# Kernel tuning notes

Measured on AMD Instinct MI355X. Metric: run time of the kernel, lower is better.

## Reference

```python
import jax, jax.numpy as jnp
import numpy as np


def _rotate_half(x):
    a, b = jnp.split(x, 2, axis=-1)
    return jnp.concatenate([-b, a], axis=-1)


def _rope_tables(L, d, dtype):
    inv = 1.0 / (10000.0 ** (jnp.arange(0, d, 2, dtype=jnp.float32) / d))
    ang = jnp.arange(L, dtype=jnp.float32)[:, None] * inv[None, :]  # (L, d/2)
    cos = jnp.repeat(jnp.cos(ang), 2, axis=-1)[None, :, None, :].astype(dtype)  # (1,L,1,d)
    sin = jnp.repeat(jnp.sin(ang), 2, axis=-1)[None, :, None, :].astype(dtype)
    return cos, sin


def setup_inputs() -> dict:
    key = jax.random.key(0)
    ks = jax.random.split(key, 7)
    B, L, D, h = 1, 1024, 768, 12
    d = D // h
    s = 0.02
    return {
        "X": jax.random.normal(ks[0], (B, L, D), jnp.float32),
        "Wq": jax.random.normal(ks[1], (D, D), jnp.float32) * s,
        "Wk": jax.random.normal(ks[2], (D, D), jnp.float32) * s,
        "Wv": jax.random.normal(ks[3], (D, D), jnp.float32) * s,
        "Wu": jax.random.normal(ks[4], (D, D), jnp.float32) * s,
        "Wg": jax.random.normal(ks[5], (3 * h, D), jnp.float32) * s,
        "Wo": jax.random.normal(ks[6], (D, D), jnp.float32) * s,
        "prior_mu": jnp.zeros((1, 1, h, d), jnp.float32),
        "prior_log_tau": jnp.zeros((1, 1, h, 1), jnp.float32),
    }


def _forward(X, Wq, Wk, Wv, Wu, Wg, Wo, prior_mu, prior_log_tau):
    B, L, D = X.shape
    h = prior_mu.shape[2]
    d = D // h
    eps = 1e-12
    # projections (torch Linear: x @ W.T, no bias)
    q = (X @ Wq.T).reshape(B, L, h, d)
    k = (X @ Wk.T).reshape(B, L, h, d)
    v = (X @ Wv.T).reshape(B, L, h, d)
    u = (X @ Wu.T).reshape(B, L, h, d)
    gate = (X @ Wg.T).reshape(B, L, h, 3)
    t = jnp.arange(1, L + 1, dtype=X.dtype).reshape(1, L, 1, 1)
    # calculate_logit (logit_type='deviation', causal)
    log_tau = jnp.exp(jnp.clip(prior_log_tau, -50.0, 30.0))
    u_sum = jnp.cumsum(u, axis=1)
    bar_u = (log_tau * prior_mu + u_sum) / (log_tau + t)
    s_i = -jnp.sum(u * bar_u, axis=-1, keepdims=True) / np.float32(np.sqrt(d))  # (B,L,h,1)
    # RoPE + L2 normalize q, k
    cos, sin = _rope_tables(L, d, X.dtype)
    q = q * cos + _rotate_half(q) * sin
    k = k * cos + _rotate_half(k) * sin
    q = q / jnp.maximum(jnp.linalg.norm(q, axis=-1, keepdims=True), eps)
    k = k / jnp.maximum(jnp.linalg.norm(k, axis=-1, keepdims=True), eps)
    # associative causal branch of compute_o
    s_max = jax.lax.stop_gradient(jnp.max(s_i, axis=1, keepdims=True))
    exp_s = jnp.exp(s_i - s_max)              # (B,L,h,1)
    E_t = jnp.cumsum(exp_s, axis=1)
    P_t = jnp.cumsum(s_i, axis=1)
    kv = jnp.einsum('blhd,blhe->blhde', k, v)  # (B,L,h,d,d)
    F_t = jnp.cumsum(exp_s[..., None] * kv, axis=1)
    G_t = jnp.cumsum(s_i[..., None] * kv, axis=1)
    H_t = jnp.cumsum(kv, axis=1)
    sig1 = jax.nn.sigmoid(gate[..., 0:1])      # (B,L,h,1)
    sigh = jax.nn.sigmoid(gate[..., 1:2])
    alpha = sigh / (E_t + eps)
    beta = (sig1 - sigh) / t
    gamma = -((beta * P_t + sigh) / t)
    M = alpha[..., None] * F_t + beta[..., None] * G_t + gamma[..., None] * H_t
    out = jnp.einsum('blhd,blhde->blhe', q, M)  # (B,L,h,d)
    # LayerNorm over head dim, eps=1e-5, no affine
    mu = jnp.mean(out, axis=-1, keepdims=True)
    var = jnp.mean(jnp.square(out - mu), axis=-1, keepdims=True)
    out = (out - mu) / jnp.sqrt(var + 1e-5)
    # output projection (dropout=0.0 -> identity)
    return out.reshape(B, L, D) @ Wo.T


def reference(X, Wq, Wk, Wv, Wu, Wg, Wo, prior_mu, prior_log_tau):
    return _forward(X, Wq, Wk, Wv, Wu, Wg, Wo, prior_mu, prior_log_tau)
```

## Files before the change

kernel.cpp:

```cpp
#include <hip/hip_runtime.h>
#include <hip/hip_bf16.h>
#include <math.h>

typedef __attribute__((ext_vector_type(8))) short bf16x8;
typedef __attribute__((ext_vector_type(4))) float f32x4;

#define SEQ 1024
#define DIM 768
#define NH 12
#define HD 64


__device__ __forceinline__ float wave_reduce_sum(float v) {
    for (int off = 1; off < 64; off <<= 1) v += __shfl_xor(v, off);
    return v;
}
__device__ __forceinline__ short f2bs(float x) {
    __hip_bfloat16 h = __float2bfloat16(x);
    return *reinterpret_cast<short*>(&h);
}
__device__ __forceinline__ float bs2f(short x) {
    __hip_bfloat16 h = *reinterpret_cast<__hip_bfloat16*>(&x);
    return (float)h;
}
__device__ __forceinline__ bf16x8 cvt8r(const float4& a, const float4& b) {
    bf16x8 r;
    r[0]=f2bs(a.x); r[1]=f2bs(a.y); r[2]=f2bs(a.z); r[3]=f2bs(a.w);
    r[4]=f2bs(b.x); r[5]=f2bs(b.y); r[6]=f2bs(b.z); r[7]=f2bs(b.w);
    return r;
}
__device__ __forceinline__ void async_copy16(const void* gptr, void* ldsbase, int lane) {
#if __has_builtin(__builtin_amdgcn_global_load_lds)
    __builtin_amdgcn_global_load_lds(
        (const __attribute__((address_space(1))) unsigned int*)gptr,
        (__attribute__((address_space(3))) unsigned int*)ldsbase, 16, 0, 0);
#else
    *(bf16x8*)((short*)ldsbase + lane*8) = *(const bf16x8*)gptr;
#endif
}

__global__ __launch_bounds__(256) void k_prep(const float* __restrict__ X,
    const float* __restrict__ Wq, const float* __restrict__ Wk,
    const float* __restrict__ Wv, const float* __restrict__ Wu,
    const float* __restrict__ Wg, const float* __restrict__ Wo,
    short* __restrict__ Xb, short* __restrict__ Wqb, short* __restrict__ Wkb,
    short* __restrict__ Wvb, short* __restrict__ Wub, short* __restrict__ Wgb,
    short* __restrict__ Wob)
{
    int seg = blockIdx.y;
    const float* src; short* dst; int n8;
    switch (seg) {
        case 0: src = X;  dst = Xb;  n8 = 98304; break;
        case 1: src = Wq; dst = Wqb; n8 = 73728; break;
        case 2: src = Wk; dst = Wkb; n8 = 73728; break;
        case 3: src = Wv; dst = Wvb; n8 = 73728; break;
        case 4: src = Wu; dst = Wub; n8 = 73728; break;
        case 5: src = Wg; dst = Wgb; n8 = 3456;  break;
        default: src = Wo; dst = Wob; n8 = 73728; break;
    }
    int i = blockIdx.x*256 + threadIdx.x;
    if (i >= n8) return;
    const float* s = src + (size_t)i*8;
    *(bf16x8*)(dst + (size_t)i*8) = cvt8r(*(const float4*)s, *(const float4*)(s + 4));
}

__global__ __launch_bounds__(256, 4) void k_proj5(const short* __restrict__ Xb,
    const short* __restrict__ Wqb, const short* __restrict__ Wkb,
    const short* __restrict__ Wvb, const short* __restrict__ Wub,
    const short* __restrict__ Wgb,
    __hip_bfloat16* __restrict__ Qb, __hip_bfloat16* __restrict__ Kb,
    __hip_bfloat16* __restrict__ Vt, __hip_bfloat16* __restrict__ Ub,
    float* __restrict__ G)
{
    int t = blockIdx.x;
    int mat, rt, ct;
    if (t < 576)      { int m3 = t/192; mat = (m3==2)?3:m3; int r = t%192; rt = r/12; ct = r%12; }
    else if (t < 768) { mat = 2; int r = t-576; rt = r/16; ct = r%16; }
    else              { mat = 4; rt = t-768; ct = 0; }

    __shared__ short lds[16384];

    int tid = threadIdx.x;
    int wv = tid>>6, lane = tid&63, g = lane>>4, n = lane&15;
    int wm = wv>>1, wn = wv&1;

    const short* Asrc; const short* Bsrc; int arow0, brow0, Brows;
    if (mat == 2) { Asrc = Wvb; Bsrc = Xb; arow0 = rt*64; brow0 = ct*64; Brows = SEQ; }
    else {
        Asrc = Xb; arow0 = rt*64; brow0 = ct*64;
        Bsrc = (mat==0)?Wqb:(mat==1)?Wkb:(mat==3)?Wub:Wgb;
        Brows = (mat==4) ? 36 : DIM;
    }

    auto dma_step = [&](int buf, int k0) {
        short* Ab = lds + buf*4096;
        short* Bb = lds + 8192 + buf*4096;
        for (int p = 0; p < 2; ++p) {
            int sbase = p*256 + wv*64;
            int s = sbase + lane;
            int r = s >> 3, c = s & 7, cl = c ^ (r & 7);
            async_copy16(Asrc + (size_t)(arow0 + r)*DIM + k0 + cl*8, Ab + sbase*8, lane);
            int gr = brow0 + r; if (gr >= Brows) gr = Brows - 1;
            async_copy16(Bsrc + (size_t)gr*DIM + k0 + cl*8, Bb + sbase*8, lane);
        }
    };

    f32x4 acc[2][2];
    for (int i=0;i<2;++i) for (int j=0;j<2;++j) acc[i][j] = (f32x4){0,0,0,0};

    dma_step(0, 0);
    for (int it = 0; it < 12; ++it) {
        __syncthreads();
        if (it < 11) dma_step(1 - (it & 1), (it + 1)*64);
        int buf = it & 1;
        const short* Ab = lds + buf*4096;
        const short* Bb = lds + 8192 + buf*4096;
        for (int ks = 0; ks < 2; ++ks) {
            int q = ks*4 + g;
            bf16x8 af[2], bfr[2];
            for (int i=0;i<2;++i)
                af[i] = *(const bf16x8*)(&Ab[((wm*32+i*16+n)*8 + (q ^ (n&7)))*8]);
            for (int j=0;j<2;++j)
                bfr[j] = *(const bf16x8*)(&Bb[((wn*32+j*16+n)*8 + (q ^ (n&7)))*8]);
            for (int i=0;i<2;++i)
                for (int j=0;j<2;++j)
                    acc[i][j] = __builtin_amdgcn_mfma_f32_16x16x32_bf16(af[i], bfr[j], acc[i][j], 0,0,0);
        }
    }
    __syncthreads();

    if (mat == 4) {
        for (int i=0;i<2;++i) for (int j=0;j<2;++j) for (int r=0;r<4;++r) {
            int row = rt*64 + wm*32 + i*16 + g*4 + r;
            int col = wn*32 + j*16 + n;
            if (col < 36) G[(size_t)row*36 + col] = acc[i][j][r];
        }
        return;
    }

    short* C = lds;
    for (int i=0;i<2;++i) for (int j=0;j<2;++j) for (int r=0;r<4;++r)
        C[(wm*32 + i*16 + g*4 + r)*64 + wn*32 + j*16 + n] = f2bs(acc[i][j][r]);
    __syncthreads();

    if (mat == 2) {
        const unsigned int* Cu = (const unsigned int*)C;
        for (int k = 0; k < 8; ++k) {
            int idx = k*256 + tid;
            int row = idx >> 5, cu = idx & 31;
            ((unsigned int*)(Vt + (size_t)(rt*64 + row)*SEQ + ct*64))[cu] = Cu[row*32 + cu];
        }
    } else if (mat == 3) {
        const unsigned int* Cu = (const unsigned int*)C;
        for (int k = 0; k < 8; ++k) {
            int idx = k*256 + tid;
            int row = idx >> 5, cu = idx & 31;
            ((unsigned int*)(Ub + ((size_t)ct*SEQ + rt*64 + row)*HD))[cu] = Cu[row*32 + cu];
        }
    } else {
        __hip_bfloat16* dst = (mat==0) ? Qb : Kb;
        int i2 = lane >> 1;
        float inv = expf((float)i2 * (-9.210340371976184f / 32.f));
        float c0, s0, C1, S1;
        sincosf((float)(rt*64 + wv*16) * inv, &s0, &c0);
        sincosf(inv, &S1, &C1);
        for (int k = 0; k < 16; ++k) {
            int row = wv*16 + k;
            int l = rt*64 + row;
            float x = bs2f(C[row*64 + lane]);
            float p = __shfl(x, lane ^ 32);
            float rot = (lane < 32) ? -p : p;
            float y = x*c0 + rot*s0;
            float nrm = wave_reduce_sum(y*y);
            y = y / fmaxf(sqrtf(nrm), 1e-12f);
            dst[((size_t)ct*SEQ + l)*HD + lane] = __float2bfloat16(y);
            float cn = c0*C1 - s0*S1;
            s0 = s0*C1 + c0*S1;
            c0 = cn;
        }
    }
}

__global__ __launch_bounds__(256) void k_si(const __hip_bfloat16* __restrict__ Ub,
    const float* __restrict__ pmu, const float* __restrict__ plt,
    float* __restrict__ si_)
{
    int T = blockIdx.x, h = blockIdx.y;
    int wv = threadIdx.x >> 6, lane = threadIdx.x & 63;
    int g = lane >> 4, n = lane & 15;
    int lbase = T*16;
    const short* ub = (const short*)Ub + (size_t)h*SEQ*HD;
    __shared__ float pbuf[4][16];

    bf16x8 a0 = *(const bf16x8*)(ub + (size_t)(lbase + n)*HD + g*8);
    bf16x8 a1 = *(const bf16x8*)(ub + (size_t)(lbase + n)*HD + 32 + g*8);

    float p[4] = {0.f, 0.f, 0.f, 0.f};

    for (int jt = wv; jt < T; jt += 4) {
        const short* br = ub + (size_t)(jt*16 + n)*HD + g*8;
        bf16x8 b0 = *(const bf16x8*)br;
        bf16x8 b1 = *(const bf16x8*)(br + 32);
        f32x4 sacc = {0.f,0.f,0.f,0.f};
        sacc = __builtin_amdgcn_mfma_f32_16x16x32_bf16(a0, b0, sacc, 0,0,0);
        sacc = __builtin_amdgcn_mfma_f32_16x16x32_bf16(a1, b1, sacc, 0,0,0);
        for (int r = 0; r < 4; ++r) p[r] += sacc[r];
    }
    if (wv == 0) {
        const short* br = ub + (size_t)(lbase + n)*HD + g*8;
        bf16x8 b0 = *(const bf16x8*)br;
        bf16x8 b1 = *(const bf16x8*)(br + 32);
        f32x4 d = {0.f,0.f,0.f,0.f};
        d = __builtin_amdgcn_mfma_f32_16x16x32_bf16(a0, b0, d, 0,0,0);
        d = __builtin_amdgcn_mfma_f32_16x16x32_bf16(a1, b1, d, 0,0,0);
        for (int r = 0; r < 4; ++r) if (n <= g*4 + r) p[r] += d[r];
    }
    if (wv == 1) {
        float ltau = expf(fminf(fmaxf(plt[h], -50.f), 30.f));
        for (int r = 0; r < 4; ++r) {
            int l = lbase + g*4 + r;
            float acc = 0.f;
            for (int c = n; c < 64; c += 16)
                acc += bs2f(ub[(size_t)l*HD + c]) * pmu[h*HD + c];
            p[r] += ltau * acc;
        }
    }
    for (int off = 1; off < 16; off <<= 1)
        for (int r = 0; r < 4; ++r) p[r] += __shfl_xor(p[r], off);
    if (n == 0)
        for (int r = 0; r < 4; ++r) pbuf[wv][g*4 + r] = p[r];
    __syncthreads();
    if (wv == 0 && n == 0) {
        float ltau = expf(fminf(fmaxf(plt[h], -50.f), 30.f));
        for (int r = 0; r < 4; ++r) {
            int row = g*4 + r, l = lbase + row;
            float tot = pbuf[0][row] + pbuf[1][row] + pbuf[2][row] + pbuf[3][row];
            si_[h*SEQ + l] = -tot * 0.125f / (ltau + (float)(l + 1));
        }
    }
}

__global__ __launch_bounds__(256) void k_attn(const __hip_bfloat16* __restrict__ Qb,
    const __hip_bfloat16* __restrict__ Kb, const __hip_bfloat16* __restrict__ Vt,
    const float* __restrict__ si_, const float* __restrict__ Gm,
    __hip_bfloat16* __restrict__ opre)
{
    int t = blockIdx.x, h = blockIdx.y;
    int tid = threadIdx.x;
    int wv = tid >> 6, lane = tid & 63;
    int g = lane >> 4, n = lane & 15;
    __shared__ short P[4][16*64];
    __shared__ float Op[4][16][64];
    __shared__ float red[4][2];
    __shared__ float ABG[3][16];
    __shared__ float smax_s;
    short* Pw = P[wv];
    int m0 = t*16;
    const float* si = si_ + h*SEQ;

    const short* qrow = (const short*)Qb + ((size_t)h*SEQ + m0 + n)*HD + g*8;
    bf16x8 qa0 = *(const bf16x8*)qrow;
    bf16x8 qa1 = *(const bf16x8*)(qrow + 32);

    float mx = -1e30f;
    for (int j = tid; j < m0 + 16; j += 256) mx = fmaxf(mx, si[j]);
    for (int off = 1; off < 64; off <<= 1) mx = fmaxf(mx, __shfl_xor(mx, off));
    if (lane == 0) red[wv][0] = mx;
    __syncthreads();
    if (tid == 0) smax_s = fmaxf(fmaxf(red[0][0], red[1][0]), fmaxf(red[2][0], red[3][0]));
    __syncthreads();
    float sm = smax_s;

    float se = 0.f, ss = 0.f;
    for (int j = tid; j < m0; j += 256) { float s = si[j]; se += expf(s - sm); ss += s; }
    se = wave_reduce_sum(se); ss = wave_reduce_sum(ss);
    __syncthreads();
    if (lane == 0) { red[wv][0] = se; red[wv][1] = ss; }
    __syncthreads();

    if (wv == 0 && lane < 16) {
        float Eb = red[0][0] + red[1][0] + red[2][0] + red[3][0];
        float Pb = red[0][1] + red[1][1] + red[2][1] + red[3][1];
        float sv = si[m0 + lane];
        float pe = expf(sv - sm), ps = sv;
        for (int off = 1; off < 16; off <<= 1) {
            float t1 = __shfl_up(pe, off), t2 = __shfl_up(ps, off);
            if (lane >= off) { pe += t1; ps += t2; }
        }
        float E = Eb + pe, Pv = Pb + ps;
        float tv = (float)(m0 + lane + 1);
        float s1 = 1.f / (1.f + expf(-Gm[(size_t)(m0 + lane)*36 + h*3 + 0]));
        float sh = 1.f / (1.f + expf(-Gm[(size_t)(m0 + lane)*36 + h*3 + 1]));
        float a = sh / (E + 1e-12f);
        float b = (s1 - sh) / tv;
        ABG[0][lane] = a;
        ABG[1][lane] = b;
        ABG[2][lane] = -((b * Pv + sh) / tv);
    }
    __syncthreads();

    float A_[4], B_[4], G_[4];
    for (int r = 0; r < 4; ++r) {
        A_[r] = ABG[0][g*4 + r]; B_[r] = ABG[1][g*4 + r]; G_[r] = ABG[2][g*4 + r];
    }
    f32x4 acco[4];
    for (int et = 0; et < 4; ++et) acco[et] = (f32x4){0.f,0.f,0.f,0.f};

    int jtmax = t >> 2;
    for (int jt = wv; jt <= jtmax; jt += 4) {
        int j0 = jt*64;
        for (int ct = 0; ct < 4; ++ct) {
            const short* krow = (const short*)Kb + ((size_t)h*SEQ + j0 + ct*16 + n)*HD + g*8;
            bf16x8 kb0 = *(const bf16x8*)krow;
            bf16x8 kb1 = *(const bf16x8*)(krow + 32);
            f32x4 sacc = {0.f,0.f,0.f,0.f};
            sacc = __builtin_amdgcn_mfma_f32_16x16x32_bf16(qa0, kb0, sacc, 0, 0, 0);
            sacc = __builtin_amdgcn_mfma_f32_16x16x32_bf16(qa1, kb1, sacc, 0, 0, 0);
            int j = j0 + ct*16 + n;
            float sj = si[j];
            float ej = expf(sj - sm);
            int chunk = ct*2 + (n>>3), e = n&7;
            for (int r = 0; r < 4; ++r) {
                int m = m0 + g*4 + r;
                float w = (j <= m) ? (A_[r]*ej + B_[r]*sj + G_[r]) : 0.f;
                int ml = g*4 + r;
                Pw[ml*64 + (chunk ^ (ml&7))*8 + e] = f2bs(w * sacc[r]);
            }
        }
        const short* vb = (const short*)Vt + (size_t)h*HD*SEQ;
        for (int et = 0; et < 4; ++et) {
            for (int sub = 0; sub < 2; ++sub) {
                int q = sub*4 + g;
                bf16x8 pa = *(const bf16x8*)(&Pw[n*64 + (q ^ (n&7))*8]);
                bf16x8 vfr = *(const bf16x8*)(vb + (size_t)(et*16 + n)*SEQ + j0 + sub*32 + g*8);
                acco[et] = __builtin_amdgcn_mfma_f32_16x16x32_bf16(pa, vfr, acco[et], 0, 0, 0);
            }
        }
    }
    for (int et = 0; et < 4; ++et)
        for (int r = 0; r < 4; ++r)
            Op[wv][g*4 + r][et*16 + n] = acco[et][r];
    __syncthreads();
    for (int rr = 0; rr < 4; ++rr) {
        int row = wv*4 + rr;
        float v = Op[0][row][lane] + Op[1][row][lane] + Op[2][row][lane] + Op[3][row][lane];
        float sm2 = wave_reduce_sum(v);
        float sq = wave_reduce_sum(v*v);
        float mu = sm2 * (1.f/64.f);
        float var = fmaxf(sq * (1.f/64.f) - mu*mu, 0.f);
        float invs = rsqrtf(var + 1e-5f);
        opre[(size_t)(m0 + row)*DIM + h*HD + lane] = __float2bfloat16((v - mu) * invs);
    }
}

__global__ __launch_bounds__(256, 4) void k_oproj(const short* __restrict__ A,
    const short* __restrict__ Wob, float* __restrict__ out)
{
    int rt = blockIdx.x, ct = blockIdx.y;
    __shared__ short lds[16384];

    int tid = threadIdx.x;
    int wv = tid>>6, lane = tid&63, g = lane>>4, n = lane&15;
    int wm = wv>>1, wn = wv&1;

    auto dma_step = [&](int buf, int k0) {
        short* Ab = lds + buf*4096;
        short* Bb = lds + 8192 + buf*4096;
        for (int p = 0; p < 2; ++p) {
            int sbase = p*256 + wv*64;
            int s = sbase + lane;
            int r = s >> 3, c = s & 7, cl = c ^ (r & 7);
            async_copy16(A + (size_t)(rt*64 + r)*DIM + k0 + cl*8, Ab + sbase*8, lane);
            async_copy16(Wob + (size_t)(ct*64 + r)*DIM + k0 + cl*8, Bb + sbase*8, lane);
        }
    };

    f32x4 acc[2][2];
    for (int i=0;i<2;++i) for (int j=0;j<2;++j) acc[i][j] = (f32x4){0,0,0,0};

    dma_step(0, 0);
    for (int it = 0; it < 12; ++it) {
        __syncthreads();
        if (it < 11) dma_step(1 - (it & 1), (it + 1)*64);
        int buf = it & 1;
        const short* Ab = lds + buf*4096;
        const short* Bb = lds + 8192 + buf*4096;
        for (int ks = 0; ks < 2; ++ks) {
            int q = ks*4 + g;
            bf16x8 af[2], bfr[2];
            for (int i=0;i<2;++i)
                af[i] = *(const bf16x8*)(&Ab[((wm*32+i*16+n)*8 + (q ^ (n&7)))*8]);
            for (int j=0;j<2;++j)
                bfr[j] = *(const bf16x8*)(&Bb[((wn*32+j*16+n)*8 + (q ^ (n&7)))*8]);
            for (int i=0;i<2;++i)
                for (int j=0;j<2;++j)
                    acc[i][j] = __builtin_amdgcn_mfma_f32_16x16x32_bf16(af[i], bfr[j], acc[i][j], 0,0,0);
        }
    }
    for (int i=0;i<2;++i) for (int j=0;j<2;++j) for (int r=0;r<4;++r) {
        int row = rt*64 + wm*32 + i*16 + g*4 + r;
        int col = ct*64 + wn*32 + j*16 + n;
        out[(size_t)row*DIM + col] = acc[i][j][r];
    }
}

extern "C" void kernel_launch(void* const* d_in, const int* in_sizes, int n_in,
                              void* d_out, int out_size, void* d_ws, size_t ws_size,
                              hipStream_t stream) {
    const float* X   = (const float*)d_in[0];
    const float* Wq  = (const float*)d_in[1];
    const float* Wk  = (const float*)d_in[2];
    const float* Wv  = (const float*)d_in[3];
    const float* Wu  = (const float*)d_in[4];
    const float* Wg  = (const float*)d_in[5];
    const float* Wo  = (const float*)d_in[6];
    const float* pmu = (const float*)d_in[7];
    const float* plt = (const float*)d_in[8];

    char* w = (char*)d_ws;
    __hip_bfloat16* Qb   = (__hip_bfloat16*)(w + 0);
    __hip_bfloat16* Kb   = (__hip_bfloat16*)(w + 1572864);
    __hip_bfloat16* Vt   = (__hip_bfloat16*)(w + 3145728);
    __hip_bfloat16* opre = (__hip_bfloat16*)(w + 4718592);
    float*          G    = (float*)(w + 6291456);
    float*          si_  = (float*)(w + 6438912);
    short*          Xb   = (short*)(w + 6684672);
    short*          Wqb  = (short*)(w + 8257536);
    short*          Wkb  = (short*)(w + 9437184);
    short*          Wvb  = (short*)(w + 10616832);
    short*          Wub  = (short*)(w + 11796480);
    short*          Wgb  = (short*)(w + 12976128);
    short*          Wob  = (short*)(w + 13031424);
    __hip_bfloat16* Ub   = (__hip_bfloat16*)d_out;
    float*          out  = (float*)d_out;

    hipLaunchKernelGGL(k_prep, dim3(384, 7), dim3(256), 0, stream,
                       X, Wq, Wk, Wv, Wu, Wg, Wo, Xb, Wqb, Wkb, Wvb, Wub, Wgb, Wob);
    hipLaunchKernelGGL(k_proj5, dim3(784), dim3(256), 0, stream,
                       Xb, Wqb, Wkb, Wvb, Wub, Wgb, Qb, Kb, Vt, Ub, G);
    hipLaunchKernelGGL(k_si, dim3(64, NH), dim3(256), 0, stream,
                       Ub, pmu, plt, si_);
    hipLaunchKernelGGL(k_attn, dim3(64, NH), dim3(256), 0, stream,
                       Qb, Kb, Vt, si_, G, opre);
    hipLaunchKernelGGL(k_oproj, dim3(16, 12), dim3(256), 0, stream,
                       (const short*)opre, Wob, out);
}
```

Before: 144.5 us.

## Compute U projection in prep kernel and merge s_i into projection launch

The U projection now runs inside the prep kernel as extra blocks that load fp32 X and Wu, convert them to bf16 in registers and do an LDS-staged MFMA GEMM. The bf16 copy of Wu is no longer stored. Because U is ready after prep, the s_i computation moves into the projection kernel as extra blocks, removing one kernel launch and its dependency gap. The cost is a heavier prep kernel with fp32 global loads and an unbalanced grid, plus LDS and launch-bounds pressure on the simple conversion blocks.

```diff
diff --git a/kernel.cpp b/kernel.cpp
--- a/kernel.cpp
+++ b/kernel.cpp
@@ -39,23 +39,86 @@
 #endif
 }
 
-__global__ __launch_bounds__(256) void k_prep(const float* __restrict__ X,
+__global__ __launch_bounds__(256, 3) void k_prep(const float* __restrict__ X,
     const float* __restrict__ Wq, const float* __restrict__ Wk,
-    const float* __restrict__ Wv, const float* __restrict__ Wu,
-    const float* __restrict__ Wg, const float* __restrict__ Wo,
+    const float* __restrict__ Wv, const float* __restrict__ Wg,
+    const float* __restrict__ Wo, const float* __restrict__ Wu,
     short* __restrict__ Xb, short* __restrict__ Wqb, short* __restrict__ Wkb,
-    short* __restrict__ Wvb, short* __restrict__ Wub, short* __restrict__ Wgb,
-    short* __restrict__ Wob)
+    short* __restrict__ Wvb, short* __restrict__ Wgb, short* __restrict__ Wob,
+    __hip_bfloat16* __restrict__ Ub)
 {
     int seg = blockIdx.y;
+    __shared__ short lds[16384];
+
+    if (seg == 6) {
+        int x = blockIdx.x;
+        if (x >= 192) return;
+        int rt = x / 12, ct = x % 12;
+        int tid = threadIdx.x;
+        int wv = tid>>6, lane = tid&63, g = lane>>4, n = lane&15;
+        int wm = wv>>1, wn = wv&1;
+
+        float4 ra[2][2], rb[2][2];
+        auto load_step = [&](int k0) {
+#pragma unroll
+            for (int p = 0; p < 2; ++p) {
+                int s = p*256 + wv*64 + lane;
+                int r = s >> 3, c = s & 7, cl = c ^ (r & 7);
+                const float* ap = X  + (size_t)(rt*64 + r)*DIM + k0 + cl*8;
+                ra[p][0] = *(const float4*)ap; ra[p][1] = *(const float4*)(ap + 4);
+                const float* bp = Wu + (size_t)(ct*64 + r)*DIM + k0 + cl*8;
+                rb[p][0] = *(const float4*)bp; rb[p][1] = *(const float4*)(bp + 4);
+            }
+        };
+        auto write_step = [&](int buf) {
+            short* Ab = lds + buf*4096;
+            short* Bb = lds + 8192 + buf*4096;
+#pragma unroll
+            for (int p = 0; p < 2; ++p) {
+                int s = p*256 + wv*64 + lane;
+                *(bf16x8*)(Ab + s*8) = cvt8r(ra[p][0], ra[p][1]);
+                *(bf16x8*)(Bb + s*8) = cvt8r(rb[p][0], rb[p][1]);
+            }
+        };
+
+        f32x4 acc[2][2];
+        for (int i=0;i<2;++i) for (int j=0;j<2;++j) acc[i][j] = (f32x4){0,0,0,0};
+
+        load_step(0); write_step(0);
+        for (int it = 0; it < 12; ++it) {
+            __syncthreads();
+            if (it < 11) load_step((it + 1)*64);
+            int buf = it & 1;
+            const short* Ab = lds + buf*4096;
+            const short* Bb = lds + 8192 + buf*4096;
+            for (int ks = 0; ks < 2; ++ks) {
+                int q = ks*4 + g;
+                bf16x8 af[2], bfr[2];
+                for (int i=0;i<2;++i)
+                    af[i] = *(const bf16x8*)(&Ab[((wm*32+i*16+n)*8 + (q ^ (n&7)))*8]);
+                for (int j=0;j<2;++j)
+                    bfr[j] = *(const bf16x8*)(&Bb[((wn*32+j*16+n)*8 + (q ^ (n&7)))*8]);
+                for (int i=0;i<2;++i)
+                    for (int j=0;j<2;++j)
+                        acc[i][j] = __builtin_amdgcn_mfma_f32_16x16x32_bf16(af[i], bfr[j], acc[i][j], 0,0,0);
+            }
+            if (it < 11) write_step(1 - (it & 1));
+        }
+        for (int i=0;i<2;++i) for (int j=0;j<2;++j) for (int r=0;r<4;++r) {
+            int row = wm*32 + i*16 + g*4 + r;
+            int col = wn*32 + j*16 + n;
+            Ub[((size_t)ct*SEQ + rt*64 + row)*HD + col] = __float2bfloat16(acc[i][j][r]);
+        }
+        return;
+    }
+
     const float* src; short* dst; int n8;
     switch (seg) {
         case 0: src = X;  dst = Xb;  n8 = 98304; break;
         case 1: src = Wq; dst = Wqb; n8 = 73728; break;
         case 2: src = Wk; dst = Wkb; n8 = 73728; break;
         case 3: src = Wv; dst = Wvb; n8 = 73728; break;
-        case 4: src = Wu; dst = Wub; n8 = 73728; break;
-        case 5: src = Wg; dst = Wgb; n8 = 3456;  break;
+        case 4: src = Wg; dst = Wgb; n8 = 3456;  break;
         default: src = Wo; dst = Wob; n8 = 73728; break;
     }
     int i = blockIdx.x*256 + threadIdx.x;
@@ -64,31 +127,87 @@
     *(bf16x8*)(dst + (size_t)i*8) = cvt8r(*(const float4*)s, *(const float4*)(s + 4));
 }
 
-__global__ __launch_bounds__(256, 4) void k_proj5(const short* __restrict__ Xb,
+__global__ __launch_bounds__(256, 4) void k_projsi(const short* __restrict__ Xb,
     const short* __restrict__ Wqb, const short* __restrict__ Wkb,
-    const short* __restrict__ Wvb, const short* __restrict__ Wub,
-    const short* __restrict__ Wgb,
+    const short* __restrict__ Wvb, const short* __restrict__ Wgb,
+    const __hip_bfloat16* __restrict__ Ub, const float* __restrict__ pmu,
+    const float* __restrict__ plt,
     __hip_bfloat16* __restrict__ Qb, __hip_bfloat16* __restrict__ Kb,
-    __hip_bfloat16* __restrict__ Vt, __hip_bfloat16* __restrict__ Ub,
-    float* __restrict__ G)
+    __hip_bfloat16* __restrict__ Vt, float* __restrict__ G,
+    float* __restrict__ si_)
 {
     int t = blockIdx.x;
-    int mat, rt, ct;
-    if (t < 576)      { int m3 = t/192; mat = (m3==2)?3:m3; int r = t%192; rt = r/12; ct = r%12; }
-    else if (t < 768) { mat = 2; int r = t-576; rt = r/16; ct = r%16; }
-    else              { mat = 4; rt = t-768; ct = 0; }
-
     __shared__ short lds[16384];
-
     int tid = threadIdx.x;
     int wv = tid>>6, lane = tid&63, g = lane>>4, n = lane&15;
+
+    if (t >= 592) {
+        int idx = t - 592;
+        int h = idx >> 6, T = idx & 63;
+        float* pbuf = (float*)lds;
+        int lbase = T*16;
+        const short* ub = (const short*)Ub + (size_t)h*SEQ*HD;
+
+        bf16x8 a0 = *(const bf16x8*)(ub + (size_t)(lbase + n)*HD + g*8);
+        bf16x8 a1 = *(const bf16x8*)(ub + (size_t)(lbase + n)*HD + 32 + g*8);
+
+        float p[4] = {0.f, 0.f, 0.f, 0.f};
+        for (int jt = wv; jt < T; jt += 4) {
+            const short* br = ub + (size_t)(jt*16 + n)*HD + g*8;
+            bf16x8 b0 = *(const bf16x8*)br;
+            bf16x8 b1 = *(const bf16x8*)(br + 32);
+            f32x4 sacc = {0.f,0.f,0.f,0.f};
+            sacc = __builtin_amdgcn_mfma_f32_16x16x32_bf16(a0, b0, sacc, 0,0,0);
+            sacc = __builtin_amdgcn_mfma_f32_16x16x32_bf16(a1, b1, sacc, 0,0,0);
+            for (int r = 0; r < 4; ++r) p[r] += sacc[r];
+        }
+        if (wv == 0) {
+            const short* br = ub + (size_t)(lbase + n)*HD + g*8;
+            bf16x8 b0 = *(const bf16x8*)br;
+            bf16x8 b1 = *(const bf16x8*)(br + 32);
+            f32x4 d = {0.f,0.f,0.f,0.f};
+            d = __builtin_amdgcn_mfma_f32_16x16x32_bf16(a0, b0, d, 0,0,0);
+            d = __builtin_amdgcn_mfma_f32_16x16x32_bf16(a1, b1, d, 0,0,0);
+            for (int r = 0; r < 4; ++r) if (n <= g*4 + r) p[r] += d[r];
+        }
+        if (wv == 1) {
+            float ltau = expf(fminf(fmaxf(plt[h], -50.f), 30.f));
+            for (int r = 0; r < 4; ++r) {
+                int l = lbase + g*4 + r;
+                float acc = 0.f;
+                for (int c = n; c < 64; c += 16)
+                    acc += bs2f(ub[(size_t)l*HD + c]) * pmu[h*HD + c];
+                p[r] += ltau * acc;
+            }
+        }
+        for (int off = 1; off < 16; off <<= 1)
+            for (int r = 0; r < 4; ++r) p[r] += __shfl_xor(p[r], off);
+        if (n == 0)
+            for (int r = 0; r < 4; ++r) pbuf[wv*16 + g*4 + r] = p[r];
+        __syncthreads();
+        if (wv == 0 && n == 0) {
+            float ltau = expf(fminf(fmaxf(plt[h], -50.f), 30.f));
+            for (int r = 0; r < 4; ++r) {
+                int row = g*4 + r, l = lbase + row;
+                float tot = pbuf[row] + pbuf[16 + row] + pbuf[32 + row] + pbuf[48 + row];
+                si_[h*SEQ + l] = -tot * 0.125f / (ltau + (float)(l + 1));
+            }
+        }
+        return;
+    }
+
+    int mat, rt, ct;
+    if (t < 384)      { mat = t/192; int r = t%192; rt = r/12; ct = r%12; }
+    else if (t < 576) { mat = 2; int r = t-384; rt = r/16; ct = r%16; }
+    else              { mat = 4; rt = t-576; ct = 0; }
+
     int wm = wv>>1, wn = wv&1;
 
     const short* Asrc; const short* Bsrc; int arow0, brow0, Brows;
     if (mat == 2) { Asrc = Wvb; Bsrc = Xb; arow0 = rt*64; brow0 = ct*64; Brows = SEQ; }
     else {
         Asrc = Xb; arow0 = rt*64; brow0 = ct*64;
-        Bsrc = (mat==0)?Wqb:(mat==1)?Wkb:(mat==3)?Wub:Wgb;
+        Bsrc = (mat==0)?Wqb:(mat==1)?Wkb:Wgb;
         Brows = (mat==4) ? 36 : DIM;
     }
 
@@ -149,13 +268,6 @@
             int idx = k*256 + tid;
             int row = idx >> 5, cu = idx & 31;
             ((unsigned int*)(Vt + (size_t)(rt*64 + row)*SEQ + ct*64))[cu] = Cu[row*32 + cu];
-        }
-    } else if (mat == 3) {
-        const unsigned int* Cu = (const unsigned int*)C;
-        for (int k = 0; k < 8; ++k) {
-            int idx = k*256 + tid;
-            int row = idx >> 5, cu = idx & 31;
-            ((unsigned int*)(Ub + ((size_t)ct*SEQ + rt*64 + row)*HD))[cu] = Cu[row*32 + cu];
         }
     } else {
         __hip_bfloat16* dst = (mat==0) ? Qb : Kb;
@@ -181,65 +293,6 @@
     }
 }
 
-__global__ __launch_bounds__(256) void k_si(const __hip_bfloat16* __restrict__ Ub,
-    const float* __restrict__ pmu, const float* __restrict__ plt,
-    float* __restrict__ si_)
-{
-    int T = blockIdx.x, h = blockIdx.y;
-    int wv = threadIdx.x >> 6, lane = threadIdx.x & 63;
-    int g = lane >> 4, n = lane & 15;
-    int lbase = T*16;
-    const short* ub = (const short*)Ub + (size_t)h*SEQ*HD;
-    __shared__ float pbuf[4][16];
-
-    bf16x8 a0 = *(const bf16x8*)(ub + (size_t)(lbase + n)*HD + g*8);
-    bf16x8 a1 = *(const bf16x8*)(ub + (size_t)(lbase + n)*HD + 32 + g*8);
-
-    float p[4] = {0.f, 0.f, 0.f, 0.f};
-
-    for (int jt = wv; jt < T; jt += 4) {
-        const short* br = ub + (size_t)(jt*16 + n)*HD + g*8;
-        bf16x8 b0 = *(const bf16x8*)br;
-        bf16x8 b1 = *(const bf16x8*)(br + 32);
-        f32x4 sacc = {0.f,0.f,0.f,0.f};
-        sacc = __builtin_amdgcn_mfma_f32_16x16x32_bf16(a0, b0, sacc, 0,0,0);
-        sacc = __builtin_amdgcn_mfma_f32_16x16x32_bf16(a1, b1, sacc, 0,0,0);
-        for (int r = 0; r < 4; ++r) p[r] += sacc[r];
-    }
-    if (wv == 0) {
-        const short* br = ub + (size_t)(lbase + n)*HD + g*8;
-        bf16x8 b0 = *(const bf16x8*)br;
-        bf16x8 b1 = *(const bf16x8*)(br + 32);
-        f32x4 d = {0.f,0.f,0.f,0.f};
-        d = __builtin_amdgcn_mfma_f32_16x16x32_bf16(a0, b0, d, 0,0,0);
-        d = __builtin_amdgcn_mfma_f32_16x16x32_bf16(a1, b1, d, 0,0,0);
-        for (int r = 0; r < 4; ++r) if (n <= g*4 + r) p[r] += d[r];
-    }
-    if (wv == 1) {
-        float ltau = expf(fminf(fmaxf(plt[h], -50.f), 30.f));
-        for (int r = 0; r < 4; ++r) {
-            int l = lbase + g*4 + r;
-            float acc = 0.f;
-            for (int c = n; c < 64; c += 16)
-                acc += bs2f(ub[(size_t)l*HD + c]) * pmu[h*HD + c];
-            p[r] += ltau * acc;
-        }
-    }
-    for (int off = 1; off < 16; off <<= 1)
-        for (int r = 0; r < 4; ++r) p[r] += __shfl_xor(p[r], off);
-    if (n == 0)
-        for (int r = 0; r < 4; ++r) pbuf[wv][g*4 + r] = p[r];
-    __syncthreads();
-    if (wv == 0 && n == 0) {
-        float ltau = expf(fminf(fmaxf(plt[h], -50.f), 30.f));
-        for (int r = 0; r < 4; ++r) {
-            int row = g*4 + r, l = lbase + row;
-            float tot = pbuf[0][row] + pbuf[1][row] + pbuf[2][row] + pbuf[3][row];
-            si_[h*SEQ + l] = -tot * 0.125f / (ltau + (float)(l + 1));
-        }
-    }
-}
-
 __global__ __launch_bounds__(256) void k_attn(const __hip_bfloat16* __restrict__ Qb,
     const __hip_bfloat16* __restrict__ Kb, const __hip_bfloat16* __restrict__ Vt,
     const float* __restrict__ si_, const float* __restrict__ Gm,
@@ -428,18 +481,15 @@
     short*          Wqb  = (short*)(w + 8257536);
     short*          Wkb  = (short*)(w + 9437184);
     short*          Wvb  = (short*)(w + 10616832);
-    short*          Wub  = (short*)(w + 11796480);
     short*          Wgb  = (short*)(w + 12976128);
     short*          Wob  = (short*)(w + 13031424);
     __hip_bfloat16* Ub   = (__hip_bfloat16*)d_out;
     float*          out  = (float*)d_out;
 
     hipLaunchKernelGGL(k_prep, dim3(384, 7), dim3(256), 0, stream,
-                       X, Wq, Wk, Wv, Wu, Wg, Wo, Xb, Wqb, Wkb, Wvb, Wub, Wgb, Wob);
-    hipLaunchKernelGGL(k_proj5, dim3(784), dim3(256), 0, stream,
-                       Xb, Wqb, Wkb, Wvb, Wub, Wgb, Qb, Kb, Vt, Ub, G);
-    hipLaunchKernelGGL(k_si, dim3(64, NH), dim3(256), 0, stream,
-                       Ub, pmu, plt, si_);
+                       X, Wq, Wk, Wv, Wg, Wo, Wu, Xb, Wqb, Wkb, Wvb, Wgb, Wob, Ub);
+    hipLaunchKernelGGL(k_projsi, dim3(1360), dim3(256), 0, stream,
+                       Xb, Wqb, Wkb, Wvb, Wgb, Ub, pmu, plt, Qb, Kb, Vt, G, si_);
     hipLaunchKernelGGL(k_attn, dim3(64, NH), dim3(256), 0, stream,
                        Qb, Kb, Vt, si_, G, opre);
     hipLaunchKernelGGL(k_oproj, dim3(16, 12), dim3(256), 0, stream,
```

After: 148.5 us. 2.7% more time.
